# Kernel optimization log

Hardware: AMD Instinct MI355X
Metric: run time of the kernel (lower is better)

## Reference

```python
import jax, jax.numpy as jnp
import numpy as np

T, H, NH, NKV, HD = 2048, 2048, 16, 4, 128
I, E, TOPK = 4096, 8, 2
EPS = 1e-5
THETA = 10000.0
NEG = -1e9


def rmsnorm(x, w):
    return x * jax.lax.rsqrt(jnp.mean(x * x, axis=-1, keepdims=True) + EPS) * w


def apply_rope(x, pos):
    # neox-style rotary: split head_dim in halves
    half = HD // 2
    inv_freq = 1.0 / (THETA ** (jnp.arange(half, dtype=jnp.float32) / half))
    f = pos.astype(jnp.float32)[:, None] * inv_freq[None, :]      # [T, half]
    cos = jnp.cos(f)[:, None, :]
    sin = jnp.sin(f)[:, None, :]
    x1, x2 = jnp.split(x, 2, axis=-1)
    return jnp.concatenate([x1 * cos - x2 * sin, x2 * cos + x1 * sin], axis=-1)


def setup_inputs() -> dict:
    key = jax.random.key(0)
    ks = jax.random.split(key, 10)
    s = 0.02
    return {
        "positions": jnp.arange(T, dtype=jnp.int32),
        "hidden_states": jax.random.normal(ks[0], (T, H), jnp.float32),
        "residual": jax.random.normal(ks[1], (T, H), jnp.float32),
        "ln1_w": jnp.ones((H,), jnp.float32),
        "ln2_w": jnp.ones((H,), jnp.float32),
        "wq": jax.random.normal(ks[2], (NH * HD, H), jnp.float32) * s,
        "wk": jax.random.normal(ks[3], (NKV * HD, H), jnp.float32) * s,
        "wv": jax.random.normal(ks[4], (NKV * HD, H), jnp.float32) * s,
        "wo": jax.random.normal(ks[5], (H, NH * HD), jnp.float32) * s,
        "gate_w": jax.random.normal(ks[6], (E, H), jnp.float32) * s,
        "w1": jax.random.normal(ks[7], (E, I, H), jnp.float32) * s,
        "w3": jax.random.normal(ks[8], (E, I, H), jnp.float32) * s,
        "w2": jax.random.normal(ks[9], (E, H, I), jnp.float32) * s,
    }


def reference(positions, hidden_states, residual, ln1_w, ln2_w,
              wq, wk, wv, wo, gate_w, w1, w3, w2):
    # fused add + input RMSNorm (vLLM RMSNorm with residual)
    x = hidden_states + residual
    residual = x
    h = rmsnorm(x, ln1_w)

    # attention: QKV proj, RoPE, GQA causal attention, o_proj
    q = (h @ wq.T).reshape(T, NH, HD)
    k = (h @ wk.T).reshape(T, NKV, HD)
    v = (h @ wv.T).reshape(T, NKV, HD)
    q = apply_rope(q, positions)
    k = apply_rope(k, positions)
    rep = NH // NKV
    k = jnp.repeat(k, rep, axis=1)  # [T, NH, HD]
    v = jnp.repeat(v, rep, axis=1)
    scores = jnp.einsum('qhd,khd->hqk', q, k) * (HD ** -0.5)
    causal = jnp.tril(jnp.ones((T, T), bool))
    scores = jnp.where(causal[None, :, :], scores, NEG)
    attn = jax.nn.softmax(scores, axis=-1)
    o = jnp.einsum('hqk,khd->qhd', attn, v).reshape(T, NH * HD)
    o = o @ wo.T

    # fused add + post-attention RMSNorm
    x = o + residual
    residual = x
    h = rmsnorm(x, ln2_w)

    # MoE: router top-k (renormalized) + SwiGLU experts
    logits = h @ gate_w.T                       # [T, E]
    probs = jax.nn.softmax(logits, axis=-1)
    top_w, top_i = jax.lax.top_k(probs, TOPK)
    top_w = top_w / jnp.sum(top_w, axis=-1, keepdims=True)
    coef = jnp.zeros((T, E), h.dtype).at[jnp.arange(T)[:, None], top_i].set(top_w)
    out = jnp.zeros_like(h)
    for e in range(E):
        g = h @ w1[e].T                          # [T, I]
        u = h @ w3[e].T
        out = out + coef[:, e:e + 1] * ((jax.nn.silu(g) * u) @ w2[e].T)
    return (out, residual)
```

## Files before the change

kernel.cpp:

```cpp
#include <hip/hip_runtime.h>
#include <hip/hip_bf16.h>
#include <math.h>


#define T_  2048
#define H_  2048
#define NH  16
#define NKV 4
#define HD  128
#define II_ 4096
#define NE  8
#define EPS 1e-5f
#define PROWS 6144

typedef __bf16 bf16x8 __attribute__((ext_vector_type(8)));
typedef float  f32x4  __attribute__((ext_vector_type(4)));
typedef unsigned short u16;

__device__ __forceinline__ u16 f2b(float f){ __bf16 b = (__bf16)f; return __builtin_bit_cast(u16, b); }
__device__ __forceinline__ float b2f(u16 u){ return (float)__builtin_bit_cast(__bf16, u); }

__device__ __forceinline__ void gll16(const void* g, void* l){
  __builtin_amdgcn_global_load_lds(
      (const __attribute__((address_space(1))) unsigned int*)g,
      (__attribute__((address_space(3))) unsigned int*)l, 16, 0, 0);
}

__device__ __forceinline__ bf16x8 cvt8(f32x4 a, f32x4 b){
  uint4 u;
  u.x = (unsigned)f2b(a[0]) | ((unsigned)f2b(a[1])<<16);
  u.y = (unsigned)f2b(a[2]) | ((unsigned)f2b(a[3])<<16);
  u.z = (unsigned)f2b(b[0]) | ((unsigned)f2b(b[1])<<16);
  u.w = (unsigned)f2b(b[2]) | ((unsigned)f2b(b[3])<<16);
  return __builtin_bit_cast(bf16x8, u);
}

__global__ __launch_bounds__(256) void mx_cvt(const float* __restrict__ s,
                                              u16* __restrict__ d, int n8)
{
  int i = blockIdx.x*256 + threadIdx.x;
  int stride = gridDim.x*256;
  for (; i < n8; i += stride){
    const f32x4* p = (const f32x4*)s + 2*(size_t)i;
    f32x4 a = p[0], b = p[1];
    uint4 u;
    u.x = (unsigned)f2b(a[0]) | ((unsigned)f2b(a[1])<<16);
    u.y = (unsigned)f2b(a[2]) | ((unsigned)f2b(a[3])<<16);
    u.z = (unsigned)f2b(b[0]) | ((unsigned)f2b(b[1])<<16);
    u.w = (unsigned)f2b(b[2]) | ((unsigned)f2b(b[3])<<16);
    ((uint4*)d)[i] = u;
  }
}

__global__ __launch_bounds__(256) void mx_cvt_split(const float* __restrict__ s,
                                                    u16* __restrict__ hi,
                                                    u16* __restrict__ lo, int n8)
{
  int i = blockIdx.x*256 + threadIdx.x;
  int stride = gridDim.x*256;
  for (; i < n8; i += stride){
    const f32x4* p = (const f32x4*)s + 2*(size_t)i;
    f32x4 a = p[0], b = p[1];
    uint4 uh, ul;
    u16 h0,h1,h2,h3;
    h0=f2b(a[0]); h1=f2b(a[1]); h2=f2b(a[2]); h3=f2b(a[3]);
    uh.x = (unsigned)h0 | ((unsigned)h1<<16);
    uh.y = (unsigned)h2 | ((unsigned)h3<<16);
    ul.x = (unsigned)f2b(a[0]-b2f(h0)) | ((unsigned)f2b(a[1]-b2f(h1))<<16);
    ul.y = (unsigned)f2b(a[2]-b2f(h2)) | ((unsigned)f2b(a[3]-b2f(h3))<<16);
    h0=f2b(b[0]); h1=f2b(b[1]); h2=f2b(b[2]); h3=f2b(b[3]);
    uh.z = (unsigned)h0 | ((unsigned)h1<<16);
    uh.w = (unsigned)h2 | ((unsigned)h3<<16);
    ul.z = (unsigned)f2b(b[0]-b2f(h0)) | ((unsigned)f2b(b[1]-b2f(h1))<<16);
    ul.w = (unsigned)f2b(b[2]-b2f(h2)) | ((unsigned)f2b(b[3]-b2f(h3))<<16);
    ((uint4*)hi)[i] = uh;
    ((uint4*)lo)[i] = ul;
  }
}

__global__ void mx_rope_table(const int* __restrict__ pos, float* __restrict__ cosT,
                              float* __restrict__ sinT)
{
  int i = blockIdx.x*256 + threadIdx.x;
  int t = i >> 6, d = i & 63;
  float inv = (float)exp(-((double)d/64.0) * 9.210340371976184);
  float f = (float)pos[t] * inv;
  cosT[i] = cosf(f); sinT[i] = sinf(f);
}

__global__ __launch_bounds__(256) void mx_addnorm(
    const float* __restrict__ a, const float* __restrict__ b,
    const float* __restrict__ gam, float* __restrict__ res_out,
    u16* __restrict__ hi, u16* __restrict__ lo,
    float* __restrict__ hf, u16* __restrict__ hbf, int* __restrict__ mz)
{
  int t = blockIdx.x, tid = threadIdx.x;
  if (mz && t == 0 && tid < 8) mz[tid] = 0;
  const float4* A4 = (const float4*)a + (size_t)t*512;
  const float4* B4 = (const float4*)b + (size_t)t*512;
  float4 va = A4[tid], vb = B4[tid];
  float4 x0; x0.x=va.x+vb.x; x0.y=va.y+vb.y; x0.z=va.z+vb.z; x0.w=va.w+vb.w;
  va = A4[tid+256]; vb = B4[tid+256];
  float4 x1; x1.x=va.x+vb.x; x1.y=va.y+vb.y; x1.z=va.z+vb.z; x1.w=va.w+vb.w;
  float ss = x0.x*x0.x + x0.y*x0.y + x0.z*x0.z + x0.w*x0.w
           + x1.x*x1.x + x1.y*x1.y + x1.z*x1.z + x1.w*x1.w;
  #pragma unroll
  for (int d=32; d; d>>=1) ss += __shfl_down(ss, d);
  __shared__ float red[4];
  if ((tid&63)==0) red[tid>>6] = ss;
  __syncthreads();
  ss = red[0]+red[1]+red[2]+red[3];
  float scale = rsqrtf(ss * (1.f/2048.f) + EPS);
  float4* R4 = (float4*)res_out + (size_t)t*512;
  R4[tid] = x0; R4[tid+256] = x1;
  const float4* G4p = (const float4*)gam;
  float4 g0 = G4p[tid], g1 = G4p[tid+256];
  float4 y0; y0.x=x0.x*scale*g0.x; y0.y=x0.y*scale*g0.y; y0.z=x0.z*scale*g0.z; y0.w=x0.w*scale*g0.w;
  float4 y1; y1.x=x1.x*scale*g1.x; y1.y=x1.y*scale*g1.y; y1.z=x1.z*scale*g1.z; y1.w=x1.w*scale*g1.w;
  if (hf){ float4* H4 = (float4*)hf + (size_t)t*512; H4[tid]=y0; H4[tid+256]=y1; }
  if (hi){
    ushort4 uh, ul;
    uh.x=f2b(y0.x); ul.x=f2b(y0.x-b2f(uh.x));
    uh.y=f2b(y0.y); ul.y=f2b(y0.y-b2f(uh.y));
    uh.z=f2b(y0.z); ul.z=f2b(y0.z-b2f(uh.z));
    uh.w=f2b(y0.w); ul.w=f2b(y0.w-b2f(uh.w));
    ((ushort4*)hi)[(size_t)t*512 + tid] = uh; ((ushort4*)lo)[(size_t)t*512 + tid] = ul;
    uh.x=f2b(y1.x); ul.x=f2b(y1.x-b2f(uh.x));
    uh.y=f2b(y1.y); ul.y=f2b(y1.y-b2f(uh.y));
    uh.z=f2b(y1.z); ul.z=f2b(y1.z-b2f(uh.z));
    uh.w=f2b(y1.w); ul.w=f2b(y1.w-b2f(uh.w));
    ((ushort4*)hi)[(size_t)t*512 + tid+256] = uh; ((ushort4*)lo)[(size_t)t*512 + tid+256] = ul;
  }
  if (hbf){
    ushort4 u0; u0.x=f2b(y0.x); u0.y=f2b(y0.y); u0.z=f2b(y0.z); u0.w=f2b(y0.w);
    ushort4 u1; u1.x=f2b(y1.x); u1.y=f2b(y1.y); u1.z=f2b(y1.z); u1.w=f2b(y1.w);
    ((ushort4*)hbf)[(size_t)t*512 + tid] = u0; ((ushort4*)hbf)[(size_t)t*512 + tid+256] = u1;
  }
}

template<int NX, int NY>
__global__ __launch_bounds__(256,2) void mx_gemm3g(
    const u16* __restrict__ Ah, const u16* __restrict__ Al,
    const u16* __restrict__ Bh, const u16* __restrict__ Bl,
    float* __restrict__ C, int ldc, int K)
{
  __shared__ u16 AhS[128*64], AlS[128*64], BhS[128*64], BlS[128*64];
  int bid = blockIdx.x;
  int xcd = bid & 7, j = bid >> 3;
  int x = j % NX, p = j / NX;
  int y = xcd + 8*p;
  int m0 = x*128, n0 = y*128;
  int tid = threadIdx.x;
  int w = tid>>6, lane = tid&63, wr = w>>1, wc = w&1, g = lane>>4, lr = lane&15;
  f32x4 acc[4][4];
  #pragma unroll
  for (int fm=0;fm<4;fm++)
    #pragma unroll
    for (int fn=0;fn<4;fn++) acc[fm][fn] = (f32x4){0.f,0.f,0.f,0.f};

  for (int k0 = 0; k0 < K; k0 += 64) {
    #pragma unroll
    for (int i=0;i<4;i++){
      int c = i*256 + tid, r = c>>3, ch = c&7;
      int sw = ((ch ^ (r&7))<<3);
      int db = (i*256 + w*64)<<3;
      gll16(Ah + (size_t)(m0+r)*K + k0 + sw, &AhS[db]);
      gll16(Al + (size_t)(m0+r)*K + k0 + sw, &AlS[db]);
      gll16(Bh + (size_t)(n0+r)*K + k0 + sw, &BhS[db]);
      gll16(Bl + (size_t)(n0+r)*K + k0 + sw, &BlS[db]);
    }
    __syncthreads();
    #pragma unroll
    for (int kk=0;kk<2;kk++){
      bf16x8 ah[4], al[4], bh[4], bl[4];
      #pragma unroll
      for (int fm=0;fm<4;fm++){
        int r = wr*64 + fm*16 + lr;
        int ch = ((kk<<2)+g) ^ (r&7);
        ah[fm] = *(const bf16x8*)(&AhS[(r<<6)+(ch<<3)]);
        al[fm] = *(const bf16x8*)(&AlS[(r<<6)+(ch<<3)]);
      }
      #pragma unroll
      for (int fn=0;fn<4;fn++){
        int r = wc*64 + fn*16 + lr;
        int ch = ((kk<<2)+g) ^ (r&7);
        bh[fn] = *(const bf16x8*)(&BhS[(r<<6)+(ch<<3)]);
        bl[fn] = *(const bf16x8*)(&BlS[(r<<6)+(ch<<3)]);
      }
      __builtin_amdgcn_s_setprio(1);
      #pragma unroll
      for (int fm=0;fm<4;fm++)
        #pragma unroll
        for (int fn=0;fn<4;fn++){
          acc[fm][fn] = __builtin_amdgcn_mfma_f32_16x16x32_bf16(ah[fm], bh[fn], acc[fm][fn],0,0,0);
          acc[fm][fn] = __builtin_amdgcn_mfma_f32_16x16x32_bf16(ah[fm], bl[fn], acc[fm][fn],0,0,0);
          acc[fm][fn] = __builtin_amdgcn_mfma_f32_16x16x32_bf16(al[fm], bh[fn], acc[fm][fn],0,0,0);
        }
      __builtin_amdgcn_s_setprio(0);
    }
    __syncthreads();
  }
  #pragma unroll
  for (int fm=0;fm<4;fm++)
    #pragma unroll
    for (int fn=0;fn<4;fn++)
      #pragma unroll
      for (int i=0;i<4;i++){
        size_t rg = (size_t)(m0 + wr*64 + fm*16 + g*4 + i);
        int cg = n0 + wc*64 + fn*16 + lr;
        C[rg*ldc + cg] = acc[fm][fn][i];
      }
}

template<int NX, int NY>
__global__ __launch_bounds__(256) void mx_gemm3(
    const u16* __restrict__ Ah, const u16* __restrict__ Al, int lda,
    const float* __restrict__ B,
    float* __restrict__ C, int ldc, int K)
{
  const int LDT = 72;
  __shared__ u16 Ash[128*LDT], Asl[128*LDT], Bsh[128*LDT], Bsl[128*LDT];
  int bid = blockIdx.x, x, y;
  if constexpr ((NY & 7) == 0) {
    int xcd = bid & 7, j = bid >> 3;
    x = j % NX; int p = j / NX;
    y = xcd + 8*p;
  } else { x = bid % NX; y = bid / NX; }
  int m0 = x*128, n0 = y*128;
  int tid = threadIdx.x;
  int w = tid>>6, lane = tid&63, wr = w>>1, wc = w&1, g = lane>>4, lr = lane&15;
  f32x4 acc[4][4];
  #pragma unroll
  for (int fm=0;fm<4;fm++)
    #pragma unroll
    for (int fn=0;fn<4;fn++) acc[fm][fn] = (f32x4){0.f,0.f,0.f,0.f};
  for (int k0 = 0; k0 < K; k0 += 64) {
    #pragma unroll
    for (int i=0;i<4;i++){
      int c = i*256 + tid, r = c>>3, ch = c&7;
      *(uint4*)(&Ash[r*LDT + ch*8]) = *(const uint4*)(Ah + (size_t)(m0+r)*lda + k0 + ch*8);
      *(uint4*)(&Asl[r*LDT + ch*8]) = *(const uint4*)(Al + (size_t)(m0+r)*lda + k0 + ch*8);
    }
    #pragma unroll
    for (int i=0;i<8;i++){
      int f = i*256 + tid, r = f>>4, c4 = f&15;
      float4 v = *(const float4*)(B + (size_t)(n0+r)*K + k0 + c4*4);
      ushort4 hv, lv;
      hv.x=f2b(v.x); lv.x=f2b(v.x-b2f(hv.x));
      hv.y=f2b(v.y); lv.y=f2b(v.y-b2f(hv.y));
      hv.z=f2b(v.z); lv.z=f2b(v.z-b2f(hv.z));
      hv.w=f2b(v.w); lv.w=f2b(v.w-b2f(hv.w));
      *(ushort4*)(&Bsh[r*LDT + c4*4]) = hv;
      *(ushort4*)(&Bsl[r*LDT + c4*4]) = lv;
    }
    __syncthreads();
    #pragma unroll
    for (int kk=0;kk<2;kk++){
      bf16x8 ah[4], al[4], bh[4], bl[4];
      #pragma unroll
      for (int fm=0;fm<4;fm++){
        int r = wr*64 + fm*16 + lr;
        ah[fm] = *(const bf16x8*)(&Ash[r*LDT + kk*32 + g*8]);
        al[fm] = *(const bf16x8*)(&Asl[r*LDT + kk*32 + g*8]);
      }
      #pragma unroll
      for (int fn=0;fn<4;fn++){
        int r = wc*64 + fn*16 + lr;
        bh[fn] = *(const bf16x8*)(&Bsh[r*LDT + kk*32 + g*8]);
        bl[fn] = *(const bf16x8*)(&Bsl[r*LDT + kk*32 + g*8]);
      }
      __builtin_amdgcn_s_setprio(1);
      #pragma unroll
      for (int fm=0;fm<4;fm++)
        #pragma unroll
        for (int fn=0;fn<4;fn++){
          acc[fm][fn] = __builtin_amdgcn_mfma_f32_16x16x32_bf16(ah[fm], bh[fn], acc[fm][fn],0,0,0);
          acc[fm][fn] = __builtin_amdgcn_mfma_f32_16x16x32_bf16(ah[fm], bl[fn], acc[fm][fn],0,0,0);
          acc[fm][fn] = __builtin_amdgcn_mfma_f32_16x16x32_bf16(al[fm], bh[fn], acc[fm][fn],0,0,0);
        }
      __builtin_amdgcn_s_setprio(0);
    }
    __syncthreads();
  }
  #pragma unroll
  for (int fm=0;fm<4;fm++)
    #pragma unroll
    for (int fn=0;fn<4;fn++)
      #pragma unroll
      for (int i=0;i<4;i++){
        size_t rg = (size_t)(m0 + wr*64 + fm*16 + g*4 + i);
        int cg = n0 + wc*64 + fn*16 + lr;
        C[rg*ldc + cg] = acc[fm][fn][i];
      }
}

template<int NY>
__global__ __launch_bounds__(256,2) void mx_moe_w13(
    const u16* __restrict__ A,
    const u16* __restrict__ B1, const u16* __restrict__ B3,
    u16* __restrict__ Y,
    const int* __restrict__ row_map, const int* __restrict__ meta)
{
  __shared__ u16 As[128*64], B1s[128*64], B3s[128*64];
  int bid = blockIdx.x;
  int xcd = bid & 7, j = bid >> 3;
  int x = j & 15, p = j >> 4;
  int panel = xcd + 8*p;
  int e = panel / NY, y = panel % NY;
  if (x >= meta[16+e]) return;
  int rowbase = meta[8+e] + (x<<7);
  const u16* B1p = B1 + ((size_t)e*II_ + y*128)*H_;
  const u16* B3p = B3 + ((size_t)e*II_ + y*128)*H_;
  int tid = threadIdx.x;
  int w = tid>>6, lane = tid&63, wr = w>>1, wc = w&1, g = lane>>4, lr = lane&15;

  f32x4 acc1[4][4], acc3[4][4];
  #pragma unroll
  for (int fm=0;fm<4;fm++)
    #pragma unroll
    for (int fn=0;fn<4;fn++){ acc1[fm][fn]=(f32x4){0,0,0,0}; acc3[fm][fn]=(f32x4){0,0,0,0}; }

  for (int k0 = 0; k0 < H_; k0 += 64) {
    #pragma unroll
    for (int i=0;i<4;i++){
      int c = i*256 + tid, r = c>>3, ch = c&7;
      int sw = (ch ^ (r&7))<<3;
      int db = (i*256 + w*64)<<3;
      int grow = row_map[rowbase + r];
      gll16(A   + (size_t)grow*H_ + k0 + sw, &As[db]);
      gll16(B1p + (size_t)r*H_    + k0 + sw, &B1s[db]);
      gll16(B3p + (size_t)r*H_    + k0 + sw, &B3s[db]);
    }
    __syncthreads();
    #pragma unroll
    for (int kk=0;kk<2;kk++){
      bf16x8 af[4], b1f[4], b3f[4];
      #pragma unroll
      for (int fm=0;fm<4;fm++){
        int r = wr*64 + fm*16 + lr;
        int ch = ((kk<<2)+g) ^ (r&7);
        af[fm] = *(const bf16x8*)(&As[(r<<6)+(ch<<3)]);
      }
      #pragma unroll
      for (int fn=0;fn<4;fn++){
        int r = wc*64 + fn*16 + lr;
        int ch = ((kk<<2)+g) ^ (r&7);
        b1f[fn] = *(const bf16x8*)(&B1s[(r<<6)+(ch<<3)]);
        b3f[fn] = *(const bf16x8*)(&B3s[(r<<6)+(ch<<3)]);
      }
      __builtin_amdgcn_s_setprio(1);
      #pragma unroll
      for (int fm=0;fm<4;fm++)
        #pragma unroll
        for (int fn=0;fn<4;fn++){
          acc1[fm][fn] = __builtin_amdgcn_mfma_f32_16x16x32_bf16(af[fm], b1f[fn], acc1[fm][fn],0,0,0);
          acc3[fm][fn] = __builtin_amdgcn_mfma_f32_16x16x32_bf16(af[fm], b3f[fn], acc3[fm][fn],0,0,0);
        }
      __builtin_amdgcn_s_setprio(0);
    }
    __syncthreads();
  }
  int n0 = y*128 + wc*64;
  #pragma unroll
  for (int fm=0;fm<4;fm++)
    #pragma unroll
    for (int fn=0;fn<4;fn++)
      #pragma unroll
      for (int i=0;i<4;i++){
        size_t rg = (size_t)(rowbase + wr*64 + fm*16 + g*4 + i);
        int cg = n0 + fn*16 + lr;
        float gg = acc1[fm][fn][i], uu = acc3[fm][fn][i];
        float sg = gg / (1.f + __expf(-gg));
        Y[rg*II_ + cg] = f2b(sg * uu);
      }
}

template<int NY>
__global__ __launch_bounds__(256,2) void mx_moe_w2k(
    const u16* __restrict__ A,
    const u16* __restrict__ B,
    float* __restrict__ C,
    const int* __restrict__ meta)
{
  __shared__ u16 As[128*64], Bs[128*64];
  int bid = blockIdx.x;
  int xcd = bid & 7, j = bid >> 3;
  int x = j & 15, p = j >> 4;
  int panel = xcd + 8*p;
  int e = panel / NY, y = panel % NY;
  if (x >= meta[16+e]) return;
  int rowbase = meta[8+e] + (x<<7);
  const u16* Bp = B + ((size_t)e*H_ + y*128)*II_;
  int tid = threadIdx.x;
  int w = tid>>6, lane = tid&63, wr = w>>1, wc = w&1, g = lane>>4, lr = lane&15;

  f32x4 acc[4][4];
  #pragma unroll
  for (int fm=0;fm<4;fm++)
    #pragma unroll
    for (int fn=0;fn<4;fn++) acc[fm][fn] = (f32x4){0,0,0,0};

  for (int k0 = 0; k0 < II_; k0 += 64) {
    #pragma unroll
    for (int i=0;i<4;i++){
      int c = i*256 + tid, r = c>>3, ch = c&7;
      int sw = (ch ^ (r&7))<<3;
      int db = (i*256 + w*64)<<3;
      gll16(A  + (size_t)(rowbase + r)*II_ + k0 + sw, &As[db]);
      gll16(Bp + (size_t)r*II_             + k0 + sw, &Bs[db]);
    }
    __syncthreads();
    #pragma unroll
    for (int kk=0;kk<2;kk++){
      bf16x8 af[4], bf[4];
      #pragma unroll
      for (int fm=0;fm<4;fm++){
        int r = wr*64 + fm*16 + lr;
        int ch = ((kk<<2)+g) ^ (r&7);
        af[fm] = *(const bf16x8*)(&As[(r<<6)+(ch<<3)]);
      }
      #pragma unroll
      for (int fn=0;fn<4;fn++){
        int r = wc*64 + fn*16 + lr;
        int ch = ((kk<<2)+g) ^ (r&7);
        bf[fn] = *(const bf16x8*)(&Bs[(r<<6)+(ch<<3)]);
      }
      __builtin_amdgcn_s_setprio(1);
      #pragma unroll
      for (int fm=0;fm<4;fm++)
        #pragma unroll
        for (int fn=0;fn<4;fn++)
          acc[fm][fn] = __builtin_amdgcn_mfma_f32_16x16x32_bf16(af[fm], bf[fn], acc[fm][fn],0,0,0);
      __builtin_amdgcn_s_setprio(0);
    }
    __syncthreads();
  }
  int n0 = y*128 + wc*64;
  #pragma unroll
  for (int fm=0;fm<4;fm++)
    #pragma unroll
    for (int fn=0;fn<4;fn++)
      #pragma unroll
      for (int i=0;i<4;i++){
        size_t rg = (size_t)(rowbase + wr*64 + fm*16 + g*4 + i);
        int cg = n0 + fn*16 + lr;
        C[rg*H_ + cg] = acc[fm][fn][i];
      }
}

__global__ __launch_bounds__(256) void mx_rope_apply(const float* __restrict__ qkv,
    const float* __restrict__ cosT, const float* __restrict__ sinT,
    u16* __restrict__ qh, u16* __restrict__ ql, u16* __restrict__ kh, u16* __restrict__ kl)
{
  int t = blockIdx.x*4 + (threadIdx.x>>6);
  int hh = blockIdx.y, d = threadIdx.x & 63;
  const float* row = qkv + (size_t)t*3072;
  float c = cosT[t*64+d], s = sinT[t*64+d];
  float x1, x2; size_t base; u16 *oh, *ol;
  if (hh < NH){ x1 = row[hh*HD+d]; x2 = row[hh*HD+d+64];
     base = ((size_t)hh*T_ + t)*HD; oh = qh; ol = ql; }
  else { int kvh = hh-NH; x1 = row[2048 + kvh*HD + d]; x2 = row[2048 + kvh*HD + d + 64];
     base = ((size_t)kvh*T_ + t)*HD; oh = kh; ol = kl; }
  float o1 = x1*c - x2*s, o2 = x2*c + x1*s;
  u16 a = f2b(o1); oh[base+d]    = a; ol[base+d]    = f2b(o1 - b2f(a));
  u16 b = f2b(o2); oh[base+d+64] = b; ol[base+d+64] = f2b(o2 - b2f(b));
}

__global__ void mx_transpose_v(const float* __restrict__ qkv,
                               u16* __restrict__ vh, u16* __restrict__ vl)
{
  __shared__ float tile[64][132];
  int kv = blockIdx.x, t0 = blockIdx.y*64, tid = threadIdx.x;
  #pragma unroll
  for (int it=0; it<32; ++it){
    int idx = it*256 + tid; int r = idx>>7, d = idx&127;
    tile[r][d] = qkv[(size_t)(t0+r)*3072 + 2560 + kv*HD + d];
  }
  __syncthreads();
  #pragma unroll
  for (int it=0; it<32; ++it){
    int idx = it*256 + tid; int d = idx>>6, j = idx&63;
    float x = tile[j][d];
    u16 a = f2b(x);
    size_t o = ((size_t)kv*HD + d)*T_ + t0 + j;
    vh[o] = a; vl[o] = f2b(x - b2f(a));
  }
}

__global__ __launch_bounds__(512) void mx_attn(
  const u16* __restrict__ qh_, const u16* __restrict__ ql_,
  const u16* __restrict__ kh_, const u16* __restrict__ kl_,
  const u16* __restrict__ vh_, const u16* __restrict__ vl_,
  u16* __restrict__ oh_, u16* __restrict__ ol_)
{
  int pair = blockIdx.y;
  int kvh = pair >> 1;
  int qt = (pair & 4) ? (31 - (int)blockIdx.x) : (int)blockIdx.x;
  int tid = threadIdx.x, w = tid>>6, lane = tid&63, g = lane>>4, lr = lane&15;
  int head = pair*2 + (w>>2);
  int q0 = qt*64 + (w&3)*16;
  __shared__ u16 KV[2][4][8192];
  __shared__ u16 Ph[8][1024], Pl[8][1024];

  bf16x8 qfh[4], qfl[4];
  const u16* qrh = qh_ + ((size_t)head*T_ + q0 + lr)*HD;
  const u16* qrl = ql_ + ((size_t)head*T_ + q0 + lr)*HD;
  #pragma unroll
  for (int kk=0;kk<4;kk++){
    qfh[kk] = *(const bf16x8*)(qrh + kk*32 + g*8);
    qfl[kk] = *(const bf16x8*)(qrl + kk*32 + g*8);
  }
  f32x4 o[8];
  #pragma unroll
  for (int nf=0;nf<8;nf++) o[nf] = (f32x4){0.f,0.f,0.f,0.f};
  float mreg[4] = {-3e38f,-3e38f,-3e38f,-3e38f}, lsum[4] = {0.f,0.f,0.f,0.f};

  const u16* kbase = kh_ + (size_t)kvh*T_*HD;
  const u16* lbase = kl_ + (size_t)kvh*T_*HD;
  const u16* vbase = vh_ + (size_t)kvh*HD*T_;
  const u16* wbase = vl_ + (size_t)kvh*HD*T_;

  auto stage = [&](int buf, int kvb){
    #pragma unroll
    for (int i=0;i<2;i++){
      int cb = i*512 + w*64;
      int c  = cb + lane;
      int kr = c>>4, kc = ((c&15) ^ (kr&7))<<3;
      gll16(kbase + (size_t)(kvb+kr)*HD + kc, &KV[buf][0][cb*8]);
      gll16(lbase + (size_t)(kvb+kr)*HD + kc, &KV[buf][1][cb*8]);
      int vr = c>>3, vc = ((c&7) ^ (vr&7))<<3;
      gll16(vbase + (size_t)vr*T_ + kvb + vc, &KV[buf][2][cb*8]);
      gll16(wbase + (size_t)vr*T_ + kvb + vc, &KV[buf][3][cb*8]);
    }
  };

  stage(0, 0);

  for (int kt = 0; kt <= qt; ++kt) {
    int cur = kt & 1;
    int kvb = kt*64;
    if (kt < qt) {
      stage(cur^1, kvb+64);
      asm volatile("s_waitcnt vmcnt(8)" ::: "memory");
    } else {
      asm volatile("s_waitcnt vmcnt(0)" ::: "memory");
    }
    __builtin_amdgcn_s_barrier();

    f32x4 s[4];
    #pragma unroll
    for (int nf=0;nf<4;nf++) s[nf] = (f32x4){0.f,0.f,0.f,0.f};
    __builtin_amdgcn_s_setprio(1);
    #pragma unroll
    for (int nf=0; nf<4; nf++){
      int row = nf*16 + lr;
      #pragma unroll
      for (int kk=0;kk<4;kk++){
        int off = row*128 + ((((kk<<2)+g) ^ (lr&7))<<3);
        bf16x8 kf = *(const bf16x8*)(&KV[cur][0][off]);
        bf16x8 kg = *(const bf16x8*)(&KV[cur][1][off]);
        s[nf] = __builtin_amdgcn_mfma_f32_16x16x32_bf16(qfh[kk], kf, s[nf],0,0,0);
        s[nf] = __builtin_amdgcn_mfma_f32_16x16x32_bf16(qfh[kk], kg, s[nf],0,0,0);
        s[nf] = __builtin_amdgcn_mfma_f32_16x16x32_bf16(qfl[kk], kf, s[nf],0,0,0);
      }
    }
    __builtin_amdgcn_s_setprio(0);

    float sv[4][4], pm[4];
    #pragma unroll
    for (int i=0;i<4;i++) pm[i] = -3e38f;
    bool diag = (kt == qt);
    #pragma unroll
    for (int nf=0;nf<4;nf++)
      #pragma unroll
      for (int i=0;i<4;i++){
        float v = s[nf][i] * 0.08838834764831845f;
        if (diag && (kvb + nf*16 + lr > q0 + g*4 + i)) v = -1e30f;
        sv[nf][i] = v;
        pm[i] = fmaxf(pm[i], v);
      }
    #pragma unroll
    for (int i=0;i<4;i++)
      #pragma unroll
      for (int d=1; d<16; d<<=1) pm[i] = fmaxf(pm[i], __shfl_xor(pm[i], d));
    float sf[4], psum[4];
    #pragma unroll
    for (int i=0;i<4;i++){
      float nm = fmaxf(mreg[i], pm[i]);
      sf[i] = __expf(mreg[i] - nm);
      mreg[i] = nm; psum[i] = 0.f;
    }
    #pragma unroll
    for (int nf=0;nf<4;nf++)
      #pragma unroll
      for (int i=0;i<4;i++){
        float e = __expf(sv[nf][i] - mreg[i]);
        sv[nf][i] = e; psum[i] += e;
      }
    #pragma unroll
    for (int i=0;i<4;i++){
      #pragma unroll
      for (int d=1; d<16; d<<=1) psum[i] += __shfl_xor(psum[i], d);
      lsum[i] = lsum[i]*sf[i] + psum[i];
    }
    #pragma unroll
    for (int nf=0;nf<8;nf++)
      #pragma unroll
      for (int i=0;i<4;i++) o[nf][i] *= sf[i];

    #pragma unroll
    for (int nf=0;nf<4;nf++)
      #pragma unroll
      for (int i=0;i<4;i++){
        int qi = g*4 + i, kv = nf*16 + lr;
        int idx = qi*64 + (kv ^ ((qi&7)<<3));
        u16 hb = f2b(sv[nf][i]);
        Ph[w][idx] = hb;
        Pl[w][idx] = f2b(sv[nf][i] - b2f(hb));
      }

    #pragma unroll
    for (int kk2=0; kk2<2; kk2++){
      int pidx = lr*64 + ((kk2*32 + g*8) ^ ((lr&7)<<3));
      bf16x8 ph = *(const bf16x8*)(&Ph[w][pidx]);
      bf16x8 pl = *(const bf16x8*)(&Pl[w][pidx]);
      __builtin_amdgcn_s_setprio(1);
      #pragma unroll
      for (int nf=0; nf<8; nf++){
        int row = nf*16 + lr;
        int off = row*64 + ((((kk2<<2)+g) ^ (lr&7))<<3);
        bf16x8 vf = *(const bf16x8*)(&KV[cur][2][off]);
        bf16x8 vg = *(const bf16x8*)(&KV[cur][3][off]);
        o[nf] = __builtin_amdgcn_mfma_f32_16x16x32_bf16(ph, vf, o[nf],0,0,0);
        o[nf] = __builtin_amdgcn_mfma_f32_16x16x32_bf16(ph, vg, o[nf],0,0,0);
        o[nf] = __builtin_amdgcn_mfma_f32_16x16x32_bf16(pl, vf, o[nf],0,0,0);
      }
      __builtin_amdgcn_s_setprio(0);
    }
    __builtin_amdgcn_s_barrier();
  }

  float inv[4];
  #pragma unroll
  for (int i=0;i<4;i++) inv[i] = 1.0f / lsum[i];
  #pragma unroll
  for (int nf=0;nf<8;nf++)
    #pragma unroll
    for (int i=0;i<4;i++){
      float v = o[nf][i] * inv[i];
      size_t oidx = (size_t)(q0 + g*4 + i)*2048 + head*HD + nf*16 + lr;
      u16 hb = f2b(v);
      oh_[oidx] = hb; ol_[oidx] = f2b(v - b2f(hb));
    }
}

__global__ __launch_bounds__(256) void mx_router(
    const float* __restrict__ h2, const float* __restrict__ gw,
    int* __restrict__ meta, int* __restrict__ tki, float* __restrict__ tkw)
{
  int t = blockIdx.x, tid = threadIdx.x;
  float p[8] = {0,0,0,0,0,0,0,0};
  const float* row = h2 + (size_t)t*H_;
  for (int i = tid; i < H_; i += 256) {
    float x = row[i];
    #pragma unroll
    for (int e=0;e<8;e++) p[e] += x * gw[e*H_ + i];
  }
  #pragma unroll
  for (int e=0;e<8;e++)
    #pragma unroll
    for (int d=32; d; d>>=1) p[e] += __shfl_down(p[e], d);
  __shared__ float red[4][8];
  int w = tid>>6;
  if ((tid&63)==0){
    #pragma unroll
    for (int e=0;e<8;e++) red[w][e] = p[e];
  }
  __syncthreads();
  if (tid==0){
    float lg[8];
    #pragma unroll
    for (int e=0;e<8;e++) lg[e] = red[0][e]+red[1][e]+red[2][e]+red[3][e];
    int e0 = 0;
    for (int e=1;e<8;e++) if (lg[e] > lg[e0]) e0 = e;
    int e1 = (e0==0)?1:0;
    for (int e=0;e<8;e++) if (e!=e0 && lg[e] > lg[e1]) e1 = e;
    float w0 = 1.f/(1.f + __expf(lg[e1]-lg[e0]));
    tki[t*2]=e0; tki[t*2+1]=e1; tkw[t*2]=w0; tkw[t*2+1]=1.f-w0;
    atomicAdd(&meta[e0],1); atomicAdd(&meta[e1],1);
  }
}

__global__ void mx_scan(int* __restrict__ meta, int* __restrict__ perm, int gsh)
{
  if (threadIdx.x == 0){
    int run = 0;
    for (int e=0;e<8;e++){
      meta[8+e] = run;
      int pt = (meta[e] + (1<<gsh) - 1) >> gsh;
      meta[16+e] = pt;
      run += pt << gsh;
      meta[24+e] = 0;
    }
  }
  for (int i = threadIdx.x; i < PROWS; i += 256) perm[i] = 0;
}

__global__ void mx_scatter(const int* __restrict__ tki, int* __restrict__ meta,
                           int* __restrict__ perm, int* __restrict__ slot)
{
  int t = blockIdx.x*256 + threadIdx.x;
  if (t >= T_) return;
  #pragma unroll
  for (int j=0;j<2;j++){
    int e = tki[t*2+j];
    int s = atomicAdd(&meta[24+e], 1);
    int pos = meta[8+e] + s;
    perm[pos] = t;
    slot[t*2+j] = pos;
  }
}

__global__ void mx_combine(const float* __restrict__ Y2, const int* __restrict__ slot,
                           const float* __restrict__ tkw, float* __restrict__ out)
{
  int t = blockIdx.x, tid = threadIdx.x;
  int s0 = slot[t*2], s1 = slot[t*2+1];
  float w0 = tkw[t*2], w1 = tkw[t*2+1];
  const float4* r0 = (const float4*)(Y2 + (size_t)s0*H_);
  const float4* r1 = (const float4*)(Y2 + (size_t)s1*H_);
  float4* o4 = (float4*)(out + (size_t)t*H_);
  for (int i = tid; i < 512; i += 256){
    float4 a = r0[i], b = r1[i], c;
    c.x = w0*a.x + w1*b.x; c.y = w0*a.y + w1*b.y;
    c.z = w0*a.z + w1*b.z; c.w = w0*a.w + w1*b.w;
    o4[i] = c;
  }
}

extern "C" void kernel_launch(void* const* d_in, const int* in_sizes, int n_in,
                              void* d_out, int out_size, void* d_ws, size_t ws_size,
                              hipStream_t stream)
{
  (void)in_sizes; (void)n_in; (void)out_size;
  const int*   positions = (const int*)  d_in[0];
  const float* hidden    = (const float*)d_in[1];
  const float* residual  = (const float*)d_in[2];
  const float* ln1       = (const float*)d_in[3];
  const float* ln2       = (const float*)d_in[4];
  const float* wq        = (const float*)d_in[5];
  const float* wk        = (const float*)d_in[6];
  const float* wv        = (const float*)d_in[7];
  const float* wo        = (const float*)d_in[8];
  const float* gatew     = (const float*)d_in[9];
  const float* w1        = (const float*)d_in[10];
  const float* w3        = (const float*)d_in[11];
  const float* w2        = (const float*)d_in[12];
  float* outp = (float*)d_out;
  char* ws = (char*)d_ws;

  size_t off = 0;
  auto alloc = [&](size_t n){ size_t o = off; off += (n + 255) & ~(size_t)255; return o; };
  float* cosT = (float*)(ws + alloc((size_t)T_*64*4));
  float* sinT = (float*)(ws + alloc((size_t)T_*64*4));
  size_t res1_off = alloc((size_t)T_*H_*4);
  float* res1 = (float*)(ws + res1_off);
  u16*   h1h  = (u16*)  (ws + alloc((size_t)T_*H_*2));
  u16*   h1l  = (u16*)  (ws + alloc((size_t)T_*H_*2));
  float* qkvF = (float*)(ws + alloc((size_t)T_*3072*4));
  size_t qh_off = alloc((size_t)NH*T_*HD*2);
  u16*   qh   = (u16*)  (ws + qh_off);
  u16*   ql   = (u16*)  (ws + alloc((size_t)NH*T_*HD*2));
  u16*   kh   = (u16*)  (ws + alloc((size_t)NKV*T_*HD*2));
  u16*   kl   = (u16*)  (ws + alloc((size_t)NKV*T_*HD*2));
  u16*   vh   = (u16*)  (ws + alloc((size_t)NKV*T_*HD*2));
  u16*   vl   = (u16*)  (ws + alloc((size_t)NKV*T_*HD*2));
  u16*   aoh  = (u16*)  (ws + alloc((size_t)T_*2048*2));
  u16*   aol  = (u16*)  (ws + alloc((size_t)T_*2048*2));
  float* oF   = (float*)(ws + alloc((size_t)T_*H_*4));
  float* h2f  = (float*)(ws + alloc((size_t)T_*H_*4));
  u16*   h2b  = (u16*)  (ws + alloc((size_t)T_*H_*2));
  int*   meta = (int*)  (ws + alloc(32*4));
  int*   tki  = (int*)  (ws + alloc((size_t)T_*2*4));
  float* tkw  = (float*)(ws + alloc((size_t)T_*2*4));
  int*   slot = (int*)  (ws + alloc((size_t)T_*2*4));
  int*   perm = (int*)  (ws + alloc((size_t)PROWS*4));
  u16*   Y1   = (u16*)  (ws + alloc((size_t)PROWS*II_*2));
  float* Y2   = (float*)(ws + qh_off);
  u16* w1b = (u16*)(ws + alloc((size_t)NE*II_*H_*2));
  u16* w3b = (u16*)(ws + alloc((size_t)NE*II_*H_*2));
  u16* w2b = (u16*)(ws + alloc((size_t)NE*H_*II_*2));
  u16* qwh = (u16*)(ws + alloc((size_t)3072*H_*2));
  u16* qwl = (u16*)(ws + alloc((size_t)3072*H_*2));
  u16* woh = (u16*)(ws + alloc((size_t)H_*H_*2));
  u16* wol = (u16*)(ws + alloc((size_t)H_*H_*2));

  int n8 = NE*II_*H_/8;
  mx_cvt<<<2048, 256, 0, stream>>>(w1, w1b, n8);
  mx_cvt<<<2048, 256, 0, stream>>>(w3, w3b, n8);
  mx_cvt<<<2048, 256, 0, stream>>>(w2, w2b, n8);
  mx_cvt_split<<<512, 256, 0, stream>>>(wq, qwh,             qwl,             2048*2048/8);
  mx_cvt_split<<<512, 256, 0, stream>>>(wk, qwh + 2048*2048, qwl + 2048*2048, 512*2048/8);
  mx_cvt_split<<<512, 256, 0, stream>>>(wv, qwh + 2560*2048, qwl + 2560*2048, 512*2048/8);
  mx_cvt_split<<<512, 256, 0, stream>>>(wo, woh,             wol,             2048*2048/8);
  mx_rope_table<<<512, 256, 0, stream>>>(positions, cosT, sinT);
  mx_addnorm<<<T_, 256, 0, stream>>>(hidden, residual, ln1, res1, h1h, h1l,
                                     nullptr, nullptr, nullptr);
  mx_gemm3g<16,24><<<384, 256, 0, stream>>>(h1h, h1l, qwh, qwl, qkvF, 3072, H_);
  mx_rope_apply<<<dim3(T_/4, NH+NKV), 256, 0, stream>>>(qkvF, cosT, sinT, qh, ql, kh, kl);
  mx_transpose_v<<<dim3(NKV, T_/64), 256, 0, stream>>>(qkvF, vh, vl);
  mx_attn<<<dim3(T_/64, 8), 512, 0, stream>>>(qh, ql, kh, kl, vh, vl, aoh, aol);
  mx_gemm3g<16,16><<<256, 256, 0, stream>>>(aoh, aol, woh, wol, oF, 2048, 2048);
  mx_addnorm<<<T_, 256, 0, stream>>>(oF, res1, ln2, outp + (size_t)T_*H_,
                                     nullptr, nullptr, h2f, h2b, meta);
  mx_router<<<T_, 256, 0, stream>>>(h2f, gatew, meta, tki, tkw);
  mx_scan<<<1, 256, 0, stream>>>(meta, perm, 7);
  mx_scatter<<<T_/256, 256, 0, stream>>>(tki, meta, perm, slot);
  mx_moe_w13<32><<<4096, 256, 0, stream>>>(h2b, w1b, w3b, Y1, perm, meta);
  mx_moe_w2k<16><<<2048, 256, 0, stream>>>(Y1, w2b, Y2, meta);
  mx_combine<<<T_, 256, 0, stream>>>(Y2, slot, tkw, outp);
  (void)ws_size;
}
```

Before: 1.026 ms.

## Fuse MoE weight bf16 conversion into attention kernel as extra blocks

Removes the three separate MoE weight conversion launches and folds that work into additional blocks of the attention kernel grid. The goal is to overlap the memory-bound weight cast with compute-bound attention and to drop launch gaps. The risk is that the conversion blocks compete with attention for bandwidth and CUs, and that the overlap is limited by block dispatch order. Dead GEMM and helper code is also deleted.

```diff
diff --git a/kernel.cpp b/kernel.cpp
--- a/kernel.cpp
+++ b/kernel.cpp
@@ -24,32 +24,6 @@
   __builtin_amdgcn_global_load_lds(
       (const __attribute__((address_space(1))) unsigned int*)g,
       (__attribute__((address_space(3))) unsigned int*)l, 16, 0, 0);
-}
-
-__device__ __forceinline__ bf16x8 cvt8(f32x4 a, f32x4 b){
-  uint4 u;
-  u.x = (unsigned)f2b(a[0]) | ((unsigned)f2b(a[1])<<16);
-  u.y = (unsigned)f2b(a[2]) | ((unsigned)f2b(a[3])<<16);
-  u.z = (unsigned)f2b(b[0]) | ((unsigned)f2b(b[1])<<16);
-  u.w = (unsigned)f2b(b[2]) | ((unsigned)f2b(b[3])<<16);
-  return __builtin_bit_cast(bf16x8, u);
-}
-
-__global__ __launch_bounds__(256) void mx_cvt(const float* __restrict__ s,
-                                              u16* __restrict__ d, int n8)
-{
-  int i = blockIdx.x*256 + threadIdx.x;
-  int stride = gridDim.x*256;
-  for (; i < n8; i += stride){
-    const f32x4* p = (const f32x4*)s + 2*(size_t)i;
-    f32x4 a = p[0], b = p[1];
-    uint4 u;
-    u.x = (unsigned)f2b(a[0]) | ((unsigned)f2b(a[1])<<16);
-    u.y = (unsigned)f2b(a[2]) | ((unsigned)f2b(a[3])<<16);
-    u.z = (unsigned)f2b(b[0]) | ((unsigned)f2b(b[1])<<16);
-    u.w = (unsigned)f2b(b[2]) | ((unsigned)f2b(b[3])<<16);
-    ((uint4*)d)[i] = u;
-  }
 }
 
 __global__ __launch_bounds__(256) void mx_cvt_split(const float* __restrict__ s,
@@ -212,88 +186,6 @@
       }
 }
 
-template<int NX, int NY>
-__global__ __launch_bounds__(256) void mx_gemm3(
-    const u16* __restrict__ Ah, const u16* __restrict__ Al, int lda,
-    const float* __restrict__ B,
-    float* __restrict__ C, int ldc, int K)
-{
-  const int LDT = 72;
-  __shared__ u16 Ash[128*LDT], Asl[128*LDT], Bsh[128*LDT], Bsl[128*LDT];
-  int bid = blockIdx.x, x, y;
-  if constexpr ((NY & 7) == 0) {
-    int xcd = bid & 7, j = bid >> 3;
-    x = j % NX; int p = j / NX;
-    y = xcd + 8*p;
-  } else { x = bid % NX; y = bid / NX; }
-  int m0 = x*128, n0 = y*128;
-  int tid = threadIdx.x;
-  int w = tid>>6, lane = tid&63, wr = w>>1, wc = w&1, g = lane>>4, lr = lane&15;
-  f32x4 acc[4][4];
-  #pragma unroll
-  for (int fm=0;fm<4;fm++)
-    #pragma unroll
-    for (int fn=0;fn<4;fn++) acc[fm][fn] = (f32x4){0.f,0.f,0.f,0.f};
-  for (int k0 = 0; k0 < K; k0 += 64) {
-    #pragma unroll
-    for (int i=0;i<4;i++){
-      int c = i*256 + tid, r = c>>3, ch = c&7;
-      *(uint4*)(&Ash[r*LDT + ch*8]) = *(const uint4*)(Ah + (size_t)(m0+r)*lda + k0 + ch*8);
-      *(uint4*)(&Asl[r*LDT + ch*8]) = *(const uint4*)(Al + (size_t)(m0+r)*lda + k0 + ch*8);
-    }
-    #pragma unroll
-    for (int i=0;i<8;i++){
-      int f = i*256 + tid, r = f>>4, c4 = f&15;
-      float4 v = *(const float4*)(B + (size_t)(n0+r)*K + k0 + c4*4);
-      ushort4 hv, lv;
-      hv.x=f2b(v.x); lv.x=f2b(v.x-b2f(hv.x));
-      hv.y=f2b(v.y); lv.y=f2b(v.y-b2f(hv.y));
-      hv.z=f2b(v.z); lv.z=f2b(v.z-b2f(hv.z));
-      hv.w=f2b(v.w); lv.w=f2b(v.w-b2f(hv.w));
-      *(ushort4*)(&Bsh[r*LDT + c4*4]) = hv;
-      *(ushort4*)(&Bsl[r*LDT + c4*4]) = lv;
-    }
-    __syncthreads();
-    #pragma unroll
-    for (int kk=0;kk<2;kk++){
-      bf16x8 ah[4], al[4], bh[4], bl[4];
-      #pragma unroll
-      for (int fm=0;fm<4;fm++){
-        int r = wr*64 + fm*16 + lr;
-        ah[fm] = *(const bf16x8*)(&Ash[r*LDT + kk*32 + g*8]);
-        al[fm] = *(const bf16x8*)(&Asl[r*LDT + kk*32 + g*8]);
-      }
-      #pragma unroll
-      for (int fn=0;fn<4;fn++){
-        int r = wc*64 + fn*16 + lr;
-        bh[fn] = *(const bf16x8*)(&Bsh[r*LDT + kk*32 + g*8]);
-        bl[fn] = *(const bf16x8*)(&Bsl[r*LDT + kk*32 + g*8]);
-      }
-      __builtin_amdgcn_s_setprio(1);
-      #pragma unroll
-      for (int fm=0;fm<4;fm++)
-        #pragma unroll
-        for (int fn=0;fn<4;fn++){
-          acc[fm][fn] = __builtin_amdgcn_mfma_f32_16x16x32_bf16(ah[fm], bh[fn], acc[fm][fn],0,0,0);
-          acc[fm][fn] = __builtin_amdgcn_mfma_f32_16x16x32_bf16(ah[fm], bl[fn], acc[fm][fn],0,0,0);
-          acc[fm][fn] = __builtin_amdgcn_mfma_f32_16x16x32_bf16(al[fm], bh[fn], acc[fm][fn],0,0,0);
-        }
-      __builtin_amdgcn_s_setprio(0);
-    }
-    __syncthreads();
-  }
-  #pragma unroll
-  for (int fm=0;fm<4;fm++)
-    #pragma unroll
-    for (int fn=0;fn<4;fn++)
-      #pragma unroll
-      for (int i=0;i<4;i++){
-        size_t rg = (size_t)(m0 + wr*64 + fm*16 + g*4 + i);
-        int cg = n0 + wc*64 + fn*16 + lr;
-        C[rg*ldc + cg] = acc[fm][fn][i];
-      }
-}
-
 template<int NY>
 __global__ __launch_bounds__(256,2) void mx_moe_w13(
     const u16* __restrict__ A,
@@ -491,8 +383,33 @@
   const u16* __restrict__ qh_, const u16* __restrict__ ql_,
   const u16* __restrict__ kh_, const u16* __restrict__ kl_,
   const u16* __restrict__ vh_, const u16* __restrict__ vl_,
-  u16* __restrict__ oh_, u16* __restrict__ ol_)
-{
+  u16* __restrict__ oh_, u16* __restrict__ ol_,
+  const float* __restrict__ w1f, const float* __restrict__ w3f,
+  const float* __restrict__ w2f,
+  u16* __restrict__ w1b, u16* __restrict__ w3b, u16* __restrict__ w2b)
+{
+  if (blockIdx.y >= 8){
+    const int n8 = NE*II_*H_/8;
+    int hb = (blockIdx.y - 8)*gridDim.x + blockIdx.x;
+    int i  = hb*512 + threadIdx.x;
+    const int stride = 3840*512;
+    for (; i < 3*n8; i += stride){
+      const float* s; u16* d; int j;
+      if (i < n8)        { s = w1f; d = w1b; j = i; }
+      else if (i < 2*n8) { s = w3f; d = w3b; j = i - n8; }
+      else               { s = w2f; d = w2b; j = i - 2*n8; }
+      const f32x4* p = (const f32x4*)s + 2*(size_t)j;
+      f32x4 a = p[0], b = p[1];
+      uint4 u;
+      u.x = (unsigned)f2b(a[0]) | ((unsigned)f2b(a[1])<<16);
+      u.y = (unsigned)f2b(a[2]) | ((unsigned)f2b(a[3])<<16);
+      u.z = (unsigned)f2b(b[0]) | ((unsigned)f2b(b[1])<<16);
+      u.w = (unsigned)f2b(b[2]) | ((unsigned)f2b(b[3])<<16);
+      ((uint4*)d)[j] = u;
+    }
+    return;
+  }
+
   int pair = blockIdx.y;
   int kvh = pair >> 1;
   int qt = (pair & 4) ? (31 - (int)blockIdx.x) : (int)blockIdx.x;
@@ -795,10 +712,6 @@
   u16* woh = (u16*)(ws + alloc((size_t)H_*H_*2));
   u16* wol = (u16*)(ws + alloc((size_t)H_*H_*2));
 
-  int n8 = NE*II_*H_/8;
-  mx_cvt<<<2048, 256, 0, stream>>>(w1, w1b, n8);
-  mx_cvt<<<2048, 256, 0, stream>>>(w3, w3b, n8);
-  mx_cvt<<<2048, 256, 0, stream>>>(w2, w2b, n8);
   mx_cvt_split<<<512, 256, 0, stream>>>(wq, qwh,             qwl,             2048*2048/8);
   mx_cvt_split<<<512, 256, 0, stream>>>(wk, qwh + 2048*2048, qwl + 2048*2048, 512*2048/8);
   mx_cvt_split<<<512, 256, 0, stream>>>(wv, qwh + 2560*2048, qwl + 2560*2048, 512*2048/8);
@@ -809,7 +722,8 @@
   mx_gemm3g<16,24><<<384, 256, 0, stream>>>(h1h, h1l, qwh, qwl, qkvF, 3072, H_);
   mx_rope_apply<<<dim3(T_/4, NH+NKV), 256, 0, stream>>>(qkvF, cosT, sinT, qh, ql, kh, kl);
   mx_transpose_v<<<dim3(NKV, T_/64), 256, 0, stream>>>(qkvF, vh, vl);
-  mx_attn<<<dim3(T_/64, 8), 512, 0, stream>>>(qh, ql, kh, kl, vh, vl, aoh, aol);
+  mx_attn<<<dim3(T_/64, 128), 512, 0, stream>>>(qh, ql, kh, kl, vh, vl, aoh, aol,
+                                                w1, w3, w2, w1b, w3b, w2b);
   mx_gemm3g<16,16><<<256, 256, 0, stream>>>(aoh, aol, woh, wol, oF, 2048, 2048);
   mx_addnorm<<<T_, 256, 0, stream>>>(oF, res1, ln2, outp + (size_t)T_*H_,
                                      nullptr, nullptr, h2f, h2b, meta);
```

After: 1.009 ms. Within noise of the previous version (-1.6%).
